# Performance work log

Measured on AMD Instinct MI355X. Metric: run time of the kernel, lower is better.

The kernel has to match this reference:

```python
import jax, jax.numpy as jnp
import numpy as np

N, K = 4096, 12          # nodes, incoming edges per node
E = N * K                # bonds
INPUT_DIM = 128
N_HEADS = 16
HEAD_DIM = 8
OUT_DIM = N_HEADS * HEAD_DIM   # 128
NUM_GAUSS = 20
NUM_ANG_FUNCS = 3              # AngularEncoding -> 1 + 3*2*2 = 13 dims
A_DIM = 1 + NUM_ANG_FUNCS * 4
KV_DIM = INPUT_DIM + 2 * NUM_GAUSS + A_DIM  # 181
Q_DIM = INPUT_DIM


def _build_graph_and_triplets():
    # edge e = i*K + t-1 : row=(i+t)%N -> col=i  (K incoming edges per node)
    col = np.repeat(np.arange(N), K)
    row = (col + np.tile(np.arange(1, K + 1), N)) % N
    bond_index = np.stack([row, col]).astype(np.int64)  # [2, E]
    # triplets: for edge e=(j->i), pair with every incoming edge (k->j) of j
    idx_ji = np.repeat(np.arange(E), K)
    idx_kj = np.repeat(row, K) * K + np.tile(np.arange(K), E)
    idx_i = col[idx_ji]
    idx_j = row[idx_ji]
    idx_k = row[idx_kj]
    mask = idx_i != idx_k
    return (bond_index, idx_i[mask], idx_j[mask], idx_k[mask],
            idx_kj[mask], idx_ji[mask])


def setup_inputs() -> dict:
    key = jax.random.key(0)
    ks = jax.random.split(key, 8)
    bond_index, idx_i, idx_j, idx_k, idx_kj, idx_ji = _build_graph_and_triplets()
    w = 0.05
    return {
        "h": jax.random.normal(ks[0], (N, INPUT_DIM), dtype=jnp.float32),
        "h_bond": jax.random.normal(ks[1], (E, INPUT_DIM), dtype=jnp.float32),
        "pos": jax.random.normal(ks[2], (N, 3), dtype=jnp.float32),
        "bond_index": jnp.asarray(bond_index),
        "idx_i": jnp.asarray(idx_i), "idx_j": jnp.asarray(idx_j),
        "idx_k": jnp.asarray(idx_k), "idx_kj": jnp.asarray(idx_kj),
        "idx_ji": jnp.asarray(idx_ji),
        "W_key": jax.random.normal(ks[3], (KV_DIM, OUT_DIM), dtype=jnp.float32) * w,
        "W_value": jax.random.normal(ks[4], (KV_DIM, OUT_DIM), dtype=jnp.float32) * w,
        "W_query": jax.random.normal(ks[5], (Q_DIM, OUT_DIM), dtype=jnp.float32) * w,
        "W_edge0": jax.random.normal(ks[6], (NUM_GAUSS, OUT_DIM), dtype=jnp.float32) * w,
        "W_edge1": jax.random.normal(ks[7], (NUM_GAUSS, OUT_DIM), dtype=jnp.float32) * w,
    }


def reference(h, h_bond, pos, bond_index, idx_i, idx_j, idx_k, idx_kj, idx_ji,
              W_key, W_value, W_query, W_edge0, W_edge1):
    Eb = h_bond.shape[0]
    row, col = bond_index[0], bond_index[1]
    # per-bond distance + Gaussian smearing (start=0, stop=10, 20 gaussians)
    dist = jnp.sqrt(jnp.sum((pos[col] - pos[row]) ** 2, axis=-1))  # [E]
    offset = jnp.linspace(0.0, 10.0, NUM_GAUSS)
    coeff = -0.5 / (offset[1] - offset[0]) ** 2
    r_feat = jnp.exp(coeff * (dist[:, None] - offset) ** 2)        # [E, 20]
    # per-triplet angle + angular encoding
    pos_i = pos[idx_i]
    pos_ji = pos[idx_j] - pos_i
    pos_ki = pos[idx_k] - pos_i
    a = jnp.sum(pos_ji * pos_ki, axis=-1)
    b = jnp.linalg.norm(jnp.cross(pos_ji, pos_ki), axis=-1)
    angle = jnp.arctan2(b, a)                                      # [T]
    t = jnp.arange(1, NUM_ANG_FUNCS + 1, dtype=jnp.float32)
    freq = jnp.concatenate([t, 1.0 / t])                           # [6]
    x = angle[:, None]
    a_feat = jnp.concatenate([x, jnp.sin(x * freq), jnp.cos(x * freq)], axis=-1)  # [T,13]
    # triplet gathers
    r_kj, r_ji = r_feat[idx_kj], r_feat[idx_ji]
    kv_input = jnp.concatenate([h_bond[idx_kj], r_kj, r_ji, a_feat], axis=-1)  # [T,181]
    q_input = h_bond[idx_ji]                                                    # [T,128]
    T = kv_input.shape[0]
    k_proj = (kv_input @ W_key).reshape(T, N_HEADS, HEAD_DIM)
    v_proj = (kv_input @ W_value).reshape(T, N_HEADS, HEAD_DIM)
    q_proj = (q_input @ W_query).reshape(T, N_HEADS, HEAD_DIM)
    edge_attn = jnp.tanh(r_ji @ W_edge0).reshape(T, N_HEADS, HEAD_DIM)
    alpha = jnp.sum(q_proj * k_proj * edge_attn, axis=-1) / np.sqrt(HEAD_DIM)   # [T,H]
    # segment softmax over idx_ji (torch_geometric softmax semantics)
    m = jax.lax.stop_gradient(jax.ops.segment_max(alpha, idx_ji, num_segments=Eb))
    ex = jnp.exp(alpha - m[idx_ji])
    s = jax.ops.segment_sum(ex, idx_ji, num_segments=Eb)
    alpha = ex / (s[idx_ji] + 1e-16)
    msg = v_proj * jnp.tanh(r_ji @ W_edge1).reshape(T, N_HEADS, HEAD_DIM)
    msg = msg * alpha[:, :, None]
    out = jax.ops.segment_sum(msg, idx_ji, num_segments=Eb)  # [E,H,D]
    return out.reshape(Eb, OUT_DIM)
```

## Files before the change

kernel.cpp:

```cpp
#include <hip/hip_runtime.h>
#include <math.h>

#define INPUT_DIM 128
#define OUT_DIM 128
#define NUM_GAUSS 20
#define NH 16
#define BM 64
#define MAXT 16
#define WPB 4
#define SCALE 0.35355339059327373f


static __device__ __forceinline__ void wave_lds_fence() {
    __asm__ volatile("s_waitcnt lgkmcnt(0)" ::: "memory");
    __builtin_amdgcn_wave_barrier();
}

__global__ __launch_bounds__(256) void rbf_kernel(
    const float* __restrict__ pos,
    const int*   __restrict__ bond_index,
    float* __restrict__ r_out,
    int E)
{
    int e = blockIdx.x * 256 + threadIdx.x;
    if (e >= E) return;
    int jrow = bond_index[e];
    int icol = bond_index[E + e];
    float dx = pos[icol*3+0] - pos[jrow*3+0];
    float dy = pos[icol*3+1] - pos[jrow*3+1];
    float dz = pos[icol*3+2] - pos[jrow*3+2];
    float dist = sqrtf(dx*dx + dy*dy + dz*dz);
    const float step = 10.f / (NUM_GAUSS - 1);
    const float coeff = -0.5f / (step * step);
    float v[NUM_GAUSS];
    #pragma unroll
    for (int g = 0; g < NUM_GAUSS; ++g) {
        float t = dist - g * step;
        v[g] = __expf(coeff * t * t);
    }
    float4* o = (float4*)&r_out[(size_t)e * NUM_GAUSS];
    #pragma unroll
    for (int q = 0; q < 5; ++q)
        o[q] = make_float4(v[4*q], v[4*q+1], v[4*q+2], v[4*q+3]);
}

__global__ __launch_bounds__(256, 3) void bond_proj_kernel(
    const float* __restrict__ h_bond,
    const float* __restrict__ r_feat,
    const float* __restrict__ Wk,
    const float* __restrict__ Wv,
    const float* __restrict__ Wq,
    const float* __restrict__ We0,
    const float* __restrict__ We1,
    float* __restrict__ KB,
    float* __restrict__ VB,
    float* __restrict__ QE,
    float* __restrict__ EA1,
    float* __restrict__ RK2,
    float* __restrict__ RV2,
    int E)
{
    __shared__ float As[BM * 148];
    const int tid = threadIdx.x;
    const int e0 = blockIdx.x * BM;

    for (int i = tid; i < BM * 32; i += 256) {
        int e = i >> 5, c = (i & 31) << 2;
        float4 v = make_float4(0.f, 0.f, 0.f, 0.f);
        if (e0 + e < E) v = *(const float4*)&h_bond[(size_t)(e0 + e) * INPUT_DIM + c];
        float* dst = &As[e * 148 + c];
        dst[0] = v.x; dst[1] = v.y; dst[2] = v.z; dst[3] = v.w;
    }
    for (int i = tid; i < BM * 5; i += 256) {
        int e = i / 5, q = (i % 5) << 2;
        float4 v = make_float4(0.f, 0.f, 0.f, 0.f);
        if (e0 + e < E) v = *(const float4*)&r_feat[(size_t)(e0 + e) * NUM_GAUSS + q];
        float* dst = &As[e * 148 + 128 + q];
        dst[0] = v.x; dst[1] = v.y; dst[2] = v.z; dst[3] = v.w;
    }
    __syncthreads();

    const int em = tid >> 5;
    const int dn = (tid & 31) << 2;
    const float* AsB = &As[em * 8 * 148];

    {
        float aK[8][4], aV[8][4], aQ[8][4], aE[8][4];
        #pragma unroll
        for (int m = 0; m < 8; ++m)
            #pragma unroll
            for (int j = 0; j < 4; ++j) { aK[m][j]=0.f; aV[m][j]=0.f; aQ[m][j]=0.f; aE[m][j]=0.f; }

        #pragma unroll 2
        for (int c = 0; c < 128; ++c) {
            float4 wk = *(const float4*)&Wk[c * OUT_DIM + dn];
            float4 wv = *(const float4*)&Wv[c * OUT_DIM + dn];
            float4 wq = *(const float4*)&Wq[c * OUT_DIM + dn];
            #pragma unroll
            for (int m = 0; m < 8; ++m) {
                float a = AsB[m * 148 + c];
                aK[m][0] = fmaf(a, wk.x, aK[m][0]); aK[m][1] = fmaf(a, wk.y, aK[m][1]);
                aK[m][2] = fmaf(a, wk.z, aK[m][2]); aK[m][3] = fmaf(a, wk.w, aK[m][3]);
                aV[m][0] = fmaf(a, wv.x, aV[m][0]); aV[m][1] = fmaf(a, wv.y, aV[m][1]);
                aV[m][2] = fmaf(a, wv.z, aV[m][2]); aV[m][3] = fmaf(a, wv.w, aV[m][3]);
                aQ[m][0] = fmaf(a, wq.x, aQ[m][0]); aQ[m][1] = fmaf(a, wq.y, aQ[m][1]);
                aQ[m][2] = fmaf(a, wq.z, aQ[m][2]); aQ[m][3] = fmaf(a, wq.w, aQ[m][3]);
            }
        }
        #pragma unroll 2
        for (int g = 0; g < 20; ++g) {
            float4 wk = *(const float4*)&Wk[(INPUT_DIM + g) * OUT_DIM + dn];
            float4 wv = *(const float4*)&Wv[(INPUT_DIM + g) * OUT_DIM + dn];
            float4 w0 = *(const float4*)&We0[g * OUT_DIM + dn];
            #pragma unroll
            for (int m = 0; m < 8; ++m) {
                float a = AsB[m * 148 + 128 + g];
                aK[m][0] = fmaf(a, wk.x, aK[m][0]); aK[m][1] = fmaf(a, wk.y, aK[m][1]);
                aK[m][2] = fmaf(a, wk.z, aK[m][2]); aK[m][3] = fmaf(a, wk.w, aK[m][3]);
                aV[m][0] = fmaf(a, wv.x, aV[m][0]); aV[m][1] = fmaf(a, wv.y, aV[m][1]);
                aV[m][2] = fmaf(a, wv.z, aV[m][2]); aV[m][3] = fmaf(a, wv.w, aV[m][3]);
                aE[m][0] = fmaf(a, w0.x, aE[m][0]); aE[m][1] = fmaf(a, w0.y, aE[m][1]);
                aE[m][2] = fmaf(a, w0.z, aE[m][2]); aE[m][3] = fmaf(a, w0.w, aE[m][3]);
            }
        }

        #pragma unroll
        for (int m = 0; m < 8; ++m) {
            int e = e0 + em * 8 + m;
            if (e < E) {
                *(float4*)&KB[(size_t)e * OUT_DIM + dn] =
                    make_float4(aK[m][0], aK[m][1], aK[m][2], aK[m][3]);
                *(float4*)&VB[(size_t)e * OUT_DIM + dn] =
                    make_float4(aV[m][0], aV[m][1], aV[m][2], aV[m][3]);
                *(float4*)&QE[(size_t)e * OUT_DIM + dn] =
                    make_float4(aQ[m][0] * tanhf(aE[m][0]), aQ[m][1] * tanhf(aE[m][1]),
                                aQ[m][2] * tanhf(aE[m][2]), aQ[m][3] * tanhf(aE[m][3]));
            }
        }
    }

    {
        float aR[8][4], aS[8][4], a1[8][4];
        #pragma unroll
        for (int m = 0; m < 8; ++m)
            #pragma unroll
            for (int j = 0; j < 4; ++j) { aR[m][j]=0.f; aS[m][j]=0.f; a1[m][j]=0.f; }

        #pragma unroll 2
        for (int g = 0; g < 20; ++g) {
            float4 wk = *(const float4*)&Wk[(148 + g) * OUT_DIM + dn];
            float4 wv = *(const float4*)&Wv[(148 + g) * OUT_DIM + dn];
            float4 w1 = *(const float4*)&We1[g * OUT_DIM + dn];
            #pragma unroll
            for (int m = 0; m < 8; ++m) {
                float a = AsB[m * 148 + 128 + g];
                aR[m][0] = fmaf(a, wk.x, aR[m][0]); aR[m][1] = fmaf(a, wk.y, aR[m][1]);
                aR[m][2] = fmaf(a, wk.z, aR[m][2]); aR[m][3] = fmaf(a, wk.w, aR[m][3]);
                aS[m][0] = fmaf(a, wv.x, aS[m][0]); aS[m][1] = fmaf(a, wv.y, aS[m][1]);
                aS[m][2] = fmaf(a, wv.z, aS[m][2]); aS[m][3] = fmaf(a, wv.w, aS[m][3]);
                a1[m][0] = fmaf(a, w1.x, a1[m][0]); a1[m][1] = fmaf(a, w1.y, a1[m][1]);
                a1[m][2] = fmaf(a, w1.z, a1[m][2]); a1[m][3] = fmaf(a, w1.w, a1[m][3]);
            }
        }
        #pragma unroll
        for (int m = 0; m < 8; ++m) {
            int e = e0 + em * 8 + m;
            if (e < E) {
                *(float4*)&RK2[(size_t)e * OUT_DIM + dn] =
                    make_float4(aR[m][0], aR[m][1], aR[m][2], aR[m][3]);
                *(float4*)&RV2[(size_t)e * OUT_DIM + dn] =
                    make_float4(aS[m][0], aS[m][1], aS[m][2], aS[m][3]);
                *(float4*)&EA1[(size_t)e * OUT_DIM + dn] =
                    make_float4(tanhf(a1[m][0]), tanhf(a1[m][1]),
                                tanhf(a1[m][2]), tanhf(a1[m][3]));
            }
        }
    }
}

__global__ __launch_bounds__(256, 2) void attn_wave_kernel(
    const float* __restrict__ pos,
    const int*   __restrict__ idx_i,
    const int*   __restrict__ idx_j,
    const int*   __restrict__ idx_k,
    const int*   __restrict__ idx_kj,
    const float* __restrict__ Wk,
    const float* __restrict__ Wv,
    const float* __restrict__ KB,
    const float* __restrict__ VB,
    const float* __restrict__ QE,
    const float* __restrict__ EA1,
    const float* __restrict__ RK2,
    const float* __restrict__ RV2,
    float* __restrict__ out,
    int E)
{
    __shared__ float afL[WPB][12][13];
    __shared__ float alphaL[WPB][12][16];

    unsigned bid = blockIdx.x, nwg = gridDim.x;
    unsigned qq = nwg >> 3, rr = nwg & 7, xc = bid & 7, rest = bid >> 3;
    unsigned swz = (xc < rr ? xc * (qq + 1) : rr * (qq + 1) + (xc - rr) * qq) + rest;

    const int l = threadIdx.x & 63;
    const int wvn = __builtin_amdgcn_readfirstlane(threadIdx.x >> 6);
    const int e = (int)swz * WPB + wvn;
    if (e >= E) return;
    const int h = l >> 2;
    const int a = l & 3;

    const int ii = idx_i[(size_t)e * 12];
    const int jj = idx_j[(size_t)e * 12];
    const float pix = pos[ii*3+0], piy = pos[ii*3+1], piz = pos[ii*3+2];
    const float jx = pos[jj*3+0]-pix, jy = pos[jj*3+1]-piy, jz = pos[jj*3+2]-piz;

    int kj = 0;
    if (l < 12) {
        int t = 12 * e + l;
        kj = idx_kj[t];
        int kk = idx_k[t];
        float kx = pos[kk*3+0]-pix, ky = pos[kk*3+1]-piy, kz = pos[kk*3+2]-piz;
        float aa = jx*kx + jy*ky + jz*kz;
        float cx = jy*kz - jz*ky, cy = jz*kx - jx*kz, cz = jx*ky - jy*kx;
        float bb = sqrtf(cx*cx + cy*cy + cz*cz);
        float ang = atan2f(bb, aa);
        float af0[13];
        af0[0] = ang;
        const float fr[6] = {1.f, 2.f, 3.f, 1.f, 0.5f, 1.f/3.f};
        #pragma unroll
        for (int q = 0; q < 6; ++q)
            __sincosf(ang * fr[q], &af0[1+q], &af0[7+q]);
        #pragma unroll
        for (int c = 0; c < 13; ++c) afL[wvn][l][c] = af0[c];
    }

    const float2 qe = *(const float2*)&QE [(size_t)e * OUT_DIM + 2*l];
    const float2 ea = *(const float2*)&EA1[(size_t)e * OUT_DIM + 2*l];
    const float2 rk = *(const float2*)&RK2[(size_t)e * OUT_DIM + 2*l];
    const float2 rv = *(const float2*)&RV2[(size_t)e * OUT_DIM + 2*l];

    float qrk2 = qe.x*rk.x + qe.y*rk.y;
    qrk2 += __shfl_xor(qrk2, 1); qrk2 += __shfl_xor(qrk2, 2);

    float qwk[13];
    #pragma unroll
    for (int c = 0; c < 13; ++c) {
        float2 w = *(const float2*)&Wk[(168 + c) * OUT_DIM + 2*l];
        float p = qe.x*w.x + qe.y*w.y;
        p += __shfl_xor(p, 1); p += __shfl_xor(p, 2);
        qwk[c] = p;
    }

    float qk3[3];
    #pragma unroll
    for (int t = 0; t < 12; ++t) {
        int kjt = __builtin_amdgcn_readlane(kj, t);
        float2 kb = *(const float2*)&KB[(size_t)kjt * OUT_DIM + 2*l];
        float v = qe.x*kb.x + qe.y*kb.y;
        v += __shfl_xor(v, 1); v += __shfl_xor(v, 2);
        if ((t & 3) == a) qk3[t >> 2] = v;
    }

    wave_lds_fence();

    float lg[3];
    #pragma unroll
    for (int q = 0; q < 3; ++q) {
        int t = a + 4*q;
        float s = 0.f;
        #pragma unroll
        for (int c = 0; c < 13; ++c) s = fmaf(afL[wvn][t][c], qwk[c], s);
        lg[q] = (qk3[q] + s + qrk2) * SCALE;
    }

    float m = fmaxf(lg[0], fmaxf(lg[1], lg[2]));
    m = fmaxf(m, __shfl_xor(m, 1)); m = fmaxf(m, __shfl_xor(m, 2));
    float ex0 = __expf(lg[0]-m), ex1 = __expf(lg[1]-m), ex2 = __expf(lg[2]-m);
    float ss = ex0 + ex1 + ex2;
    ss += __shfl_xor(ss, 1); ss += __shfl_xor(ss, 2);
    float inv = 1.f / (ss + 1e-16f);
    float al0 = ex0*inv, al1 = ex1*inv, al2 = ex2*inv;
    float Sh = ss * inv;

    alphaL[wvn][a    ][h] = al0;
    alphaL[wvn][a + 4][h] = al1;
    alphaL[wvn][a + 8][h] = al2;

    float waf[13];
    #pragma unroll
    for (int c = 0; c < 13; ++c) {
        float wp = al0*afL[wvn][a][c] + al1*afL[wvn][a+4][c] + al2*afL[wvn][a+8][c];
        wp += __shfl_xor(wp, 1); wp += __shfl_xor(wp, 2);
        waf[c] = wp;
    }

    wave_lds_fence();

    float accx = 0.f, accy = 0.f;
    #pragma unroll
    for (int t = 0; t < 12; ++t) {
        int kjt = __builtin_amdgcn_readlane(kj, t);
        float2 vb = *(const float2*)&VB[(size_t)kjt * OUT_DIM + 2*l];
        float alt = alphaL[wvn][t][h];
        accx = fmaf(alt, vb.x, accx);
        accy = fmaf(alt, vb.y, accy);
    }
    float vAx = 0.f, vAy = 0.f;
    #pragma unroll
    for (int c = 0; c < 13; ++c) {
        float2 w = *(const float2*)&Wv[(168 + c) * OUT_DIM + 2*l];
        vAx = fmaf(waf[c], w.x, vAx);
        vAy = fmaf(waf[c], w.y, vAy);
    }
    float2 o;
    o.x = ea.x * (accx + vAx + rv.x * Sh);
    o.y = ea.y * (accy + vAy + rv.y * Sh);
    *(float2*)&out[(size_t)e * OUT_DIM + 2*l] = o;
}

__global__ __launch_bounds__(128) void attn_generic_kernel(
    const float* __restrict__ pos,
    const int*   __restrict__ idx_i,
    const int*   __restrict__ idx_j,
    const int*   __restrict__ idx_k,
    const int*   __restrict__ idx_kj,
    const int*   __restrict__ idx_ji,
    const float* __restrict__ Wk,
    const float* __restrict__ Wv,
    const float* __restrict__ We1,
    const float* __restrict__ r_feat,
    const float* __restrict__ KB,
    const float* __restrict__ VB,
    const float* __restrict__ QE,
    float* __restrict__ out,
    int E, int T)
{
    __shared__ float rs[NUM_GAUSS];
    __shared__ float af[MAXT][13];
    __shared__ float logit[MAXT][NH];
    __shared__ float qwk[NH][13];
    __shared__ float waf[NH][13];
    __shared__ int   kjs[MAXT];
    __shared__ float qrk2s[NH];
    __shared__ float Shs[NH];

    const int e = blockIdx.x;
    const int d = threadIdx.x;
    const int h8 = d >> 3;

    int l = 0, hi = T;
    while (l < hi) { int mid = (l + hi) >> 1; if (idx_ji[mid] < e) l = mid + 1; else hi = mid; }
    int lo = l, c2 = 0;
    while (lo + c2 < T && c2 < MAXT && idx_ji[lo + c2] == e) ++c2;
    int cnt = c2;

    if (d < NUM_GAUSS) rs[d] = r_feat[(size_t)e * NUM_GAUSS + d];
    if (d < cnt) {
        int t = lo + d;
        kjs[d] = idx_kj[t];
        int ii = idx_i[t], jj = idx_j[t], kk = idx_k[t];
        float pix = pos[ii*3+0], piy = pos[ii*3+1], piz = pos[ii*3+2];
        float jx = pos[jj*3+0]-pix, jy = pos[jj*3+1]-piy, jz = pos[jj*3+2]-piz;
        float kx = pos[kk*3+0]-pix, ky = pos[kk*3+1]-piy, kz = pos[kk*3+2]-piz;
        float aa = jx*kx + jy*ky + jz*kz;
        float cx = jy*kz - jz*ky, cy = jz*kx - jx*kz, cz = jx*ky - jy*kx;
        float bb = sqrtf(cx*cx + cy*cy + cz*cz);
        float ang = atan2f(bb, aa);
        af[d][0] = ang;
        const float fr[6] = {1.f, 2.f, 3.f, 1.f, 0.5f, 1.f/3.f};
        #pragma unroll
        for (int q = 0; q < 6; ++q) {
            float s, cc;
            __sincosf(ang * fr[q], &s, &cc);
            af[d][1 + q] = s;
            af[d][7 + q] = cc;
        }
    }
    __syncthreads();

    const float qe = QE[(size_t)e * OUT_DIM + d];
    float s1 = 0.f, sk = 0.f, sv = 0.f;
    #pragma unroll
    for (int g = 0; g < NUM_GAUSS; ++g) {
        float rg = rs[g];
        s1 = fmaf(rg, We1[g * OUT_DIM + d], s1);
        sk = fmaf(rg, Wk[(148 + g) * OUT_DIM + d], sk);
        sv = fmaf(rg, Wv[(148 + g) * OUT_DIM + d], sv);
    }
    const float ea1 = tanhf(s1);
    const float rv2 = sv;

    {
        float v = qe * sk;
        v += __shfl_xor(v, 1, 8); v += __shfl_xor(v, 2, 8); v += __shfl_xor(v, 4, 8);
        if ((d & 7) == 0) qrk2s[h8] = v;
    }
    {
        float p[13];
        #pragma unroll
        for (int c = 0; c < 13; ++c) p[c] = qe * Wk[(168 + c) * OUT_DIM + d];
        #pragma unroll
        for (int c = 0; c < 13; ++c) {
            float v = p[c];
            v += __shfl_xor(v, 1, 8); v += __shfl_xor(v, 2, 8); v += __shfl_xor(v, 4, 8);
            if ((d & 7) == 0) qwk[h8][c] = v;
        }
    }
    for (int t = 0; t < cnt; ++t) {
        float lv = qe * KB[(size_t)kjs[t] * OUT_DIM + d];
        lv += __shfl_xor(lv, 1, 8); lv += __shfl_xor(lv, 2, 8); lv += __shfl_xor(lv, 4, 8);
        if ((d & 7) == 0) logit[t][h8] = lv;
    }
    __syncthreads();
    {
        const int hh = d & 15;
        for (int t = d >> 4; t < cnt; t += 8) {
            float s = 0.f;
            #pragma unroll
            for (int c = 0; c < 13; ++c) s = fmaf(af[t][c], qwk[hh][c], s);
            logit[t][hh] = (logit[t][hh] + s + qrk2s[hh]) * SCALE;
        }
    }
    __syncthreads();
    if (d < NH) {
        float m = -1e30f;
        for (int t = 0; t < cnt; ++t) m = fmaxf(m, logit[t][d]);
        float s = 0.f;
        for (int t = 0; t < cnt; ++t) { float ex = __expf(logit[t][d] - m); logit[t][d] = ex; s += ex; }
        float inv = 1.f / (s + 1e-16f);
        for (int t = 0; t < cnt; ++t) logit[t][d] *= inv;
        Shs[d] = s * inv;
    }
    __syncthreads();
    {
        const int hh = d & 15;
        int c = d >> 4;
        float w1 = 0.f;
        for (int t = 0; t < cnt; ++t) w1 = fmaf(logit[t][hh], af[t][c], w1);
        waf[hh][c] = w1;
        c += 8;
        if (c < 13) {
            float w2 = 0.f;
            for (int t = 0; t < cnt; ++t) w2 = fmaf(logit[t][hh], af[t][c], w2);
            waf[hh][c] = w2;
        }
    }
    __syncthreads();
    float vA = 0.f;
    #pragma unroll
    for (int c = 0; c < 13; ++c) vA = fmaf(waf[h8][c], Wv[(168 + c) * OUT_DIM + d], vA);
    float acc = 0.f;
    for (int t = 0; t < cnt; ++t)
        acc = fmaf(logit[t][h8], VB[(size_t)kjs[t] * OUT_DIM + d], acc);
    out[(size_t)e * OUT_DIM + d] = ea1 * (acc + vA + rv2 * Shs[h8]);
}

extern "C" void kernel_launch(void* const* d_in, const int* in_sizes, int n_in,
                              void* d_out, int out_size, void* d_ws, size_t ws_size,
                              hipStream_t stream) {
    const float* h_bond = (const float*)d_in[1];
    const float* pos    = (const float*)d_in[2];
    const int*   bidx   = (const int*)d_in[3];
    const int*   idx_i  = (const int*)d_in[4];
    const int*   idx_j  = (const int*)d_in[5];
    const int*   idx_k  = (const int*)d_in[6];
    const int*   idx_kj = (const int*)d_in[7];
    const int*   idx_ji = (const int*)d_in[8];
    const float* Wk     = (const float*)d_in[9];
    const float* Wv     = (const float*)d_in[10];
    const float* Wq     = (const float*)d_in[11];
    const float* We0    = (const float*)d_in[12];
    const float* We1    = (const float*)d_in[13];

    const int E = in_sizes[1] / INPUT_DIM;
    const int T = in_sizes[4];

    float* ws = (float*)d_ws;
    float* r_feat = ws;
    float* KB  = r_feat + (size_t)E * NUM_GAUSS;
    float* VB  = KB  + (size_t)E * OUT_DIM;
    float* QE  = VB  + (size_t)E * OUT_DIM;
    float* EA1 = QE  + (size_t)E * OUT_DIM;
    float* RK2 = EA1 + (size_t)E * OUT_DIM;
    float* RV2 = RK2 + (size_t)E * OUT_DIM;

    rbf_kernel<<<(E + 255) / 256, 256, 0, stream>>>(pos, bidx, r_feat, E);

    bond_proj_kernel<<<(E + BM - 1) / BM, 256, 0, stream>>>(
        h_bond, r_feat, Wk, Wv, Wq, We0, We1, KB, VB, QE, EA1, RK2, RV2, E);

    if (T == E * 12) {
        attn_wave_kernel<<<(E + WPB - 1) / WPB, 64 * WPB, 0, stream>>>(
            pos, idx_i, idx_j, idx_k, idx_kj,
            Wk, Wv, KB, VB, QE, EA1, RK2, RV2, (float*)d_out, E);
    } else {
        attn_generic_kernel<<<E, 128, 0, stream>>>(
            pos, idx_i, idx_j, idx_k, idx_kj, idx_ji,
            Wk, Wv, We1, r_feat, KB, VB, QE, (float*)d_out, E, T);
    }
}
```

Baseline: 183.9 us.

## Split r_ji edge projections into separate kernel, precompute per-head q·rk and ea*rv

Moves the r_ji-based projections (Wk/Wv rows 148-167 and We1) out of bond_proj_kernel into a new redge_kernel. That kernel reduces the q·RK2 dot product to a per-head scalar QRK2 and folds tanh(edge1) into the RV term, producing ERV. The attention kernel then reads one float per head instead of a full RK2 row, and skips the shuffle reduction. This cuts workspace traffic, but adds a kernel launch and a re-read of QE.

Result: slower. 192.9 us (+4.9%).

```diff
diff --git a/kernel.cpp b/kernel.cpp
--- a/kernel.cpp
+++ b/kernel.cpp
@@ -51,13 +51,9 @@
     const float* __restrict__ Wv,
     const float* __restrict__ Wq,
     const float* __restrict__ We0,
-    const float* __restrict__ We1,
     float* __restrict__ KB,
     float* __restrict__ VB,
     float* __restrict__ QE,
-    float* __restrict__ EA1,
-    float* __restrict__ RK2,
-    float* __restrict__ RV2,
     int E)
 {
     __shared__ float As[BM * 148];
@@ -84,96 +80,147 @@
     const int dn = (tid & 31) << 2;
     const float* AsB = &As[em * 8 * 148];
 
+    float aK[8][4], aV[8][4], aQ[8][4], aE[8][4];
+    #pragma unroll
+    for (int m = 0; m < 8; ++m)
+        #pragma unroll
+        for (int j = 0; j < 4; ++j) { aK[m][j]=0.f; aV[m][j]=0.f; aQ[m][j]=0.f; aE[m][j]=0.f; }
+
+    #pragma unroll 2
+    for (int c = 0; c < 128; ++c) {
+        float4 wk = *(const float4*)&Wk[c * OUT_DIM + dn];
+        float4 wv = *(const float4*)&Wv[c * OUT_DIM + dn];
+        float4 wq = *(const float4*)&Wq[c * OUT_DIM + dn];
+        #pragma unroll
+        for (int m = 0; m < 8; ++m) {
+            float a = AsB[m * 148 + c];
+            aK[m][0] = fmaf(a, wk.x, aK[m][0]); aK[m][1] = fmaf(a, wk.y, aK[m][1]);
+            aK[m][2] = fmaf(a, wk.z, aK[m][2]); aK[m][3] = fmaf(a, wk.w, aK[m][3]);
+            aV[m][0] = fmaf(a, wv.x, aV[m][0]); aV[m][1] = fmaf(a, wv.y, aV[m][1]);
+            aV[m][2] = fmaf(a, wv.z, aV[m][2]); aV[m][3] = fmaf(a, wv.w, aV[m][3]);
+            aQ[m][0] = fmaf(a, wq.x, aQ[m][0]); aQ[m][1] = fmaf(a, wq.y, aQ[m][1]);
+            aQ[m][2] = fmaf(a, wq.z, aQ[m][2]); aQ[m][3] = fmaf(a, wq.w, aQ[m][3]);
+        }
+    }
+    #pragma unroll 2
+    for (int g = 0; g < 20; ++g) {
+        float4 wk = *(const float4*)&Wk[(INPUT_DIM + g) * OUT_DIM + dn];
+        float4 wv = *(const float4*)&Wv[(INPUT_DIM + g) * OUT_DIM + dn];
+        float4 w0 = *(const float4*)&We0[g * OUT_DIM + dn];
+        #pragma unroll
+        for (int m = 0; m < 8; ++m) {
+            float a = AsB[m * 148 + 128 + g];
+            aK[m][0] = fmaf(a, wk.x, aK[m][0]); aK[m][1] = fmaf(a, wk.y, aK[m][1]);
+            aK[m][2] = fmaf(a, wk.z, aK[m][2]); aK[m][3] = fmaf(a, wk.w, aK[m][3]);
+            aV[m][0] = fmaf(a, wv.x, aV[m][0]); aV[m][1] = fmaf(a, wv.y, aV[m][1]);
+            aV[m][2] = fmaf(a, wv.z, aV[m][2]); aV[m][3] = fmaf(a, wv.w, aV[m][3]);
+            aE[m][0] = fmaf(a, w0.x, aE[m][0]); aE[m][1] = fmaf(a, w0.y, aE[m][1]);
+            aE[m][2] = fmaf(a, w0.z, aE[m][2]); aE[m][3] = fmaf(a, w0.w, aE[m][3]);
+        }
+    }
+
+    #pragma unroll
+    for (int m = 0; m < 8; ++m) {
+        int e = e0 + em * 8 + m;
+        if (e < E) {
+            *(float4*)&KB[(size_t)e * OUT_DIM + dn] =
+                make_float4(aK[m][0], aK[m][1], aK[m][2], aK[m][3]);
+            *(float4*)&VB[(size_t)e * OUT_DIM + dn] =
+                make_float4(aV[m][0], aV[m][1], aV[m][2], aV[m][3]);
+            *(float4*)&QE[(size_t)e * OUT_DIM + dn] =
+                make_float4(aQ[m][0] * tanhf(aE[m][0]), aQ[m][1] * tanhf(aE[m][1]),
+                            aQ[m][2] * tanhf(aE[m][2]), aQ[m][3] * tanhf(aE[m][3]));
+        }
+    }
+}
+
+__global__ __launch_bounds__(256) void redge_kernel(
+    const float* __restrict__ r_feat,
+    const float* __restrict__ QE,
+    const float* __restrict__ Wk,
+    const float* __restrict__ Wv,
+    const float* __restrict__ We1,
+    float* __restrict__ EA1,
+    float* __restrict__ ERV,
+    float* __restrict__ QRK2,
+    int E)
+{
+    __shared__ float Rs[BM][NUM_GAUSS];
+    const int tid = threadIdx.x;
+    const int e0 = blockIdx.x * BM;
+
+    for (int i = tid; i < BM * 5; i += 256) {
+        int e = i / 5, q = (i % 5) << 2;
+        float4 v = make_float4(0.f, 0.f, 0.f, 0.f);
+        if (e0 + e < E) v = *(const float4*)&r_feat[(size_t)(e0 + e) * NUM_GAUSS + q];
+        Rs[e][q] = v.x; Rs[e][q+1] = v.y; Rs[e][q+2] = v.z; Rs[e][q+3] = v.w;
+    }
+    __syncthreads();
+
+    const int em = tid >> 5;
+    const int dn = (tid & 31) << 2;
+
     {
-        float aK[8][4], aV[8][4], aQ[8][4], aE[8][4];
+        float a1[8][4], aS[8][4];
         #pragma unroll
         for (int m = 0; m < 8; ++m)
             #pragma unroll
-            for (int j = 0; j < 4; ++j) { aK[m][j]=0.f; aV[m][j]=0.f; aQ[m][j]=0.f; aE[m][j]=0.f; }
+            for (int j = 0; j < 4; ++j) { a1[m][j] = 0.f; aS[m][j] = 0.f; }
 
         #pragma unroll 2
-        for (int c = 0; c < 128; ++c) {
-            float4 wk = *(const float4*)&Wk[c * OUT_DIM + dn];
-            float4 wv = *(const float4*)&Wv[c * OUT_DIM + dn];
-            float4 wq = *(const float4*)&Wq[c * OUT_DIM + dn];
+        for (int g = 0; g < 20; ++g) {
+            float4 w1 = *(const float4*)&We1[g * OUT_DIM + dn];
+            float4 wv = *(const float4*)&Wv[(148 + g) * OUT_DIM + dn];
             #pragma unroll
             for (int m = 0; m < 8; ++m) {
-                float a = AsB[m * 148 + c];
-                aK[m][0] = fmaf(a, wk.x, aK[m][0]); aK[m][1] = fmaf(a, wk.y, aK[m][1]);
-                aK[m][2] = fmaf(a, wk.z, aK[m][2]); aK[m][3] = fmaf(a, wk.w, aK[m][3]);
-                aV[m][0] = fmaf(a, wv.x, aV[m][0]); aV[m][1] = fmaf(a, wv.y, aV[m][1]);
-                aV[m][2] = fmaf(a, wv.z, aV[m][2]); aV[m][3] = fmaf(a, wv.w, aV[m][3]);
-                aQ[m][0] = fmaf(a, wq.x, aQ[m][0]); aQ[m][1] = fmaf(a, wq.y, aQ[m][1]);
-                aQ[m][2] = fmaf(a, wq.z, aQ[m][2]); aQ[m][3] = fmaf(a, wq.w, aQ[m][3]);
+                float a = Rs[em * 8 + m][g];
+                a1[m][0] = fmaf(a, w1.x, a1[m][0]); a1[m][1] = fmaf(a, w1.y, a1[m][1]);
+                a1[m][2] = fmaf(a, w1.z, a1[m][2]); a1[m][3] = fmaf(a, w1.w, a1[m][3]);
+                aS[m][0] = fmaf(a, wv.x, aS[m][0]); aS[m][1] = fmaf(a, wv.y, aS[m][1]);
+                aS[m][2] = fmaf(a, wv.z, aS[m][2]); aS[m][3] = fmaf(a, wv.w, aS[m][3]);
             }
         }
-        #pragma unroll 2
-        for (int g = 0; g < 20; ++g) {
-            float4 wk = *(const float4*)&Wk[(INPUT_DIM + g) * OUT_DIM + dn];
-            float4 wv = *(const float4*)&Wv[(INPUT_DIM + g) * OUT_DIM + dn];
-            float4 w0 = *(const float4*)&We0[g * OUT_DIM + dn];
-            #pragma unroll
-            for (int m = 0; m < 8; ++m) {
-                float a = AsB[m * 148 + 128 + g];
-                aK[m][0] = fmaf(a, wk.x, aK[m][0]); aK[m][1] = fmaf(a, wk.y, aK[m][1]);
-                aK[m][2] = fmaf(a, wk.z, aK[m][2]); aK[m][3] = fmaf(a, wk.w, aK[m][3]);
-                aV[m][0] = fmaf(a, wv.x, aV[m][0]); aV[m][1] = fmaf(a, wv.y, aV[m][1]);
-                aV[m][2] = fmaf(a, wv.z, aV[m][2]); aV[m][3] = fmaf(a, wv.w, aV[m][3]);
-                aE[m][0] = fmaf(a, w0.x, aE[m][0]); aE[m][1] = fmaf(a, w0.y, aE[m][1]);
-                aE[m][2] = fmaf(a, w0.z, aE[m][2]); aE[m][3] = fmaf(a, w0.w, aE[m][3]);
-            }
-        }
-
         #pragma unroll
         for (int m = 0; m < 8; ++m) {
             int e = e0 + em * 8 + m;
             if (e < E) {
-                *(float4*)&KB[(size_t)e * OUT_DIM + dn] =
-                    make_float4(aK[m][0], aK[m][1], aK[m][2], aK[m][3]);
-                *(float4*)&VB[(size_t)e * OUT_DIM + dn] =
-                    make_float4(aV[m][0], aV[m][1], aV[m][2], aV[m][3]);
-                *(float4*)&QE[(size_t)e * OUT_DIM + dn] =
-                    make_float4(aQ[m][0] * tanhf(aE[m][0]), aQ[m][1] * tanhf(aE[m][1]),
-                                aQ[m][2] * tanhf(aE[m][2]), aQ[m][3] * tanhf(aE[m][3]));
+                float t0 = tanhf(a1[m][0]), t1 = tanhf(a1[m][1]);
+                float t2 = tanhf(a1[m][2]), t3 = tanhf(a1[m][3]);
+                *(float4*)&EA1[(size_t)e * OUT_DIM + dn] = make_float4(t0, t1, t2, t3);
+                *(float4*)&ERV[(size_t)e * OUT_DIM + dn] =
+                    make_float4(t0 * aS[m][0], t1 * aS[m][1], t2 * aS[m][2], t3 * aS[m][3]);
             }
         }
     }
 
     {
-        float aR[8][4], aS[8][4], a1[8][4];
+        float aR[8][4];
         #pragma unroll
         for (int m = 0; m < 8; ++m)
             #pragma unroll
-            for (int j = 0; j < 4; ++j) { aR[m][j]=0.f; aS[m][j]=0.f; a1[m][j]=0.f; }
+            for (int j = 0; j < 4; ++j) aR[m][j] = 0.f;
 
         #pragma unroll 2
         for (int g = 0; g < 20; ++g) {
             float4 wk = *(const float4*)&Wk[(148 + g) * OUT_DIM + dn];
-            float4 wv = *(const float4*)&Wv[(148 + g) * OUT_DIM + dn];
-            float4 w1 = *(const float4*)&We1[g * OUT_DIM + dn];
             #pragma unroll
             for (int m = 0; m < 8; ++m) {
-                float a = AsB[m * 148 + 128 + g];
+                float a = Rs[em * 8 + m][g];
                 aR[m][0] = fmaf(a, wk.x, aR[m][0]); aR[m][1] = fmaf(a, wk.y, aR[m][1]);
                 aR[m][2] = fmaf(a, wk.z, aR[m][2]); aR[m][3] = fmaf(a, wk.w, aR[m][3]);
-                aS[m][0] = fmaf(a, wv.x, aS[m][0]); aS[m][1] = fmaf(a, wv.y, aS[m][1]);
-                aS[m][2] = fmaf(a, wv.z, aS[m][2]); aS[m][3] = fmaf(a, wv.w, aS[m][3]);
-                a1[m][0] = fmaf(a, w1.x, a1[m][0]); a1[m][1] = fmaf(a, w1.y, a1[m][1]);
-                a1[m][2] = fmaf(a, w1.z, a1[m][2]); a1[m][3] = fmaf(a, w1.w, a1[m][3]);
             }
         }
+        const int hh = (tid & 31) >> 1;
         #pragma unroll
         for (int m = 0; m < 8; ++m) {
             int e = e0 + em * 8 + m;
+            float s = 0.f;
             if (e < E) {
-                *(float4*)&RK2[(size_t)e * OUT_DIM + dn] =
-                    make_float4(aR[m][0], aR[m][1], aR[m][2], aR[m][3]);
-                *(float4*)&RV2[(size_t)e * OUT_DIM + dn] =
-                    make_float4(aS[m][0], aS[m][1], aS[m][2], aS[m][3]);
-                *(float4*)&EA1[(size_t)e * OUT_DIM + dn] =
-                    make_float4(tanhf(a1[m][0]), tanhf(a1[m][1]),
-                                tanhf(a1[m][2]), tanhf(a1[m][3]));
+                float4 q = *(const float4*)&QE[(size_t)e * OUT_DIM + dn];
+                s = q.x*aR[m][0] + q.y*aR[m][1] + q.z*aR[m][2] + q.w*aR[m][3];
             }
+            s += __shfl_xor(s, 1);
+            if ((tid & 1) == 0 && e < E) QRK2[(size_t)e * NH + hh] = s;
         }
     }
 }
@@ -190,8 +237,8 @@
     const float* __restrict__ VB,
     const float* __restrict__ QE,
     const float* __restrict__ EA1,
-    const float* __restrict__ RK2,
-    const float* __restrict__ RV2,
+    const float* __restrict__ ERV,
+    const float* __restrict__ QRK2,
     float* __restrict__ out,
     int E)
 {
@@ -234,13 +281,10 @@
         for (int c = 0; c < 13; ++c) afL[wvn][l][c] = af0[c];
     }
 
-    const float2 qe = *(const float2*)&QE [(size_t)e * OUT_DIM + 2*l];
-    const float2 ea = *(const float2*)&EA1[(size_t)e * OUT_DIM + 2*l];
-    const float2 rk = *(const float2*)&RK2[(size_t)e * OUT_DIM + 2*l];
-    const float2 rv = *(const float2*)&RV2[(size_t)e * OUT_DIM + 2*l];
-
-    float qrk2 = qe.x*rk.x + qe.y*rk.y;
-    qrk2 += __shfl_xor(qrk2, 1); qrk2 += __shfl_xor(qrk2, 2);
+    const float2 qe  = *(const float2*)&QE [(size_t)e * OUT_DIM + 2*l];
+    const float2 ea  = *(const float2*)&EA1[(size_t)e * OUT_DIM + 2*l];
+    const float2 erv = *(const float2*)&ERV[(size_t)e * OUT_DIM + 2*l];
+    const float qrk2 = QRK2[(size_t)e * NH + h];
 
     float qwk[13];
     #pragma unroll
@@ -313,8 +357,8 @@
         vAy = fmaf(waf[c], w.y, vAy);
     }
     float2 o;
-    o.x = ea.x * (accx + vAx + rv.x * Sh);
-    o.y = ea.y * (accy + vAy + rv.y * Sh);
+    o.x = ea.x * (accx + vAx) + erv.x * Sh;
+    o.y = ea.y * (accy + vAy) + erv.y * Sh;
     *(float2*)&out[(size_t)e * OUT_DIM + 2*l] = o;
 }
 
@@ -477,22 +521,25 @@
 
     float* ws = (float*)d_ws;
     float* r_feat = ws;
-    float* KB  = r_feat + (size_t)E * NUM_GAUSS;
-    float* VB  = KB  + (size_t)E * OUT_DIM;
-    float* QE  = VB  + (size_t)E * OUT_DIM;
-    float* EA1 = QE  + (size_t)E * OUT_DIM;
-    float* RK2 = EA1 + (size_t)E * OUT_DIM;
-    float* RV2 = RK2 + (size_t)E * OUT_DIM;
+    float* KB   = r_feat + (size_t)E * NUM_GAUSS;
+    float* VB   = KB   + (size_t)E * OUT_DIM;
+    float* QE   = VB   + (size_t)E * OUT_DIM;
+    float* EA1  = QE   + (size_t)E * OUT_DIM;
+    float* ERV  = EA1  + (size_t)E * OUT_DIM;
+    float* QRK2 = ERV  + (size_t)E * OUT_DIM;
 
     rbf_kernel<<<(E + 255) / 256, 256, 0, stream>>>(pos, bidx, r_feat, E);
 
     bond_proj_kernel<<<(E + BM - 1) / BM, 256, 0, stream>>>(
-        h_bond, r_feat, Wk, Wv, Wq, We0, We1, KB, VB, QE, EA1, RK2, RV2, E);
+        h_bond, r_feat, Wk, Wv, Wq, We0, KB, VB, QE, E);
+
+    redge_kernel<<<(E + BM - 1) / BM, 256, 0, stream>>>(
+        r_feat, QE, Wk, Wv, We1, EA1, ERV, QRK2, E);
 
     if (T == E * 12) {
         attn_wave_kernel<<<(E + WPB - 1) / WPB, 64 * WPB, 0, stream>>>(
             pos, idx_i, idx_j, idx_k, idx_kj,
-            Wk, Wv, KB, VB, QE, EA1, RK2, RV2, (float*)d_out, E);
+            Wk, Wv, KB, VB, QE, EA1, ERV, QRK2, (float*)d_out, E);
     } else {
         attn_generic_kernel<<<E, 128, 0, stream>>>(
             pos, idx_i, idx_j, idx_k, idx_kj, idx_ji,
```
